# Performance work log

Measured on AMD Instinct MI355X. Metric: run time of the kernel, lower is better.

## Reference

```python
import jax, jax.numpy as jnp
import numpy as np

D_STATE = 512
D_MODEL = 512
BATCH = 8
SEQ = 4096
DT_MIN, DT_MAX = 1e-3, 0.1
LN_EPS = 1e-5


def setup_inputs() -> dict:
    key = jax.random.key(0)
    ks = jax.random.split(key, 4)
    x = jax.random.normal(ks[0], (BATCH, SEQ, D_MODEL), dtype=jnp.float32)
    volatility_scale = jax.random.uniform(ks[1], (BATCH, SEQ, 1), dtype=jnp.float32)
    # parameters (mirroring the torch module's __init__)
    log_lambda_real = jnp.linspace(np.log(DT_MIN), np.log(DT_MAX), D_STATE).astype(jnp.float32)
    log_b = jax.random.uniform(ks[2], (D_STATE, 1), dtype=jnp.float32, minval=-0.5, maxval=0.5)
    c = jax.random.normal(ks[3], (1, D_STATE), dtype=jnp.float32) / np.sqrt(D_STATE)
    log_d = jnp.zeros((1,), jnp.float32)
    ts = np.array([1.0 / 24.0, 1.0, 5.0, 21.0, 63.0], np.float32)
    extra = np.linspace(63.0, 189.0, D_STATE - len(ts), dtype=np.float32)
    log_step = jnp.log(jnp.asarray(np.concatenate([ts, extra])))
    volatility_gate = jnp.ones((D_MODEL,), jnp.float32)
    alpha = jnp.asarray(0.7, jnp.float32)
    ln_weight = jnp.ones((D_STATE,), jnp.float32)
    ln_bias = jnp.zeros((D_STATE,), jnp.float32)
    return dict(x=x, volatility_scale=volatility_scale,
                log_lambda_real=log_lambda_real, log_b=log_b, c=c, log_d=log_d,
                log_step=log_step, volatility_gate=volatility_gate, alpha=alpha,
                ln_weight=ln_weight, ln_bias=ln_bias)


def reference(x, volatility_scale, log_lambda_real, log_b, c, log_d,
              log_step, volatility_gate, alpha, ln_weight, ln_bias):
    lam = -jnp.exp(log_lambda_real)              # [N], negative real poles
    step = jnp.exp(log_step)                     # [N], per-state timescale
    b = jnp.exp(log_b)[:, 0]                     # [N]
    d = jnp.exp(log_d)                           # [1], skip gain
    # bilinear (Tustin) discretization, paired per state
    z = step * lam                               # [N]
    a_disc = (2.0 + z) / (2.0 - z)               # [N]
    b_disc = step * (1.0 + a_disc) * b / 2.0     # [N]
    gate = jax.nn.sigmoid(volatility_gate)       # [D]
    c_vec = c[0]                                 # [N]

    def layer_norm(h):
        mu = jnp.mean(h, axis=-1, keepdims=True)
        var = jnp.var(h, axis=-1, keepdims=True)
        return (h - mu) * jax.lax.rsqrt(var + LN_EPS) * ln_weight + ln_bias

    def scan_step(h, inp):
        x_t, v_t = inp                           # [B,D], [B,1]
        h = a_disc * h + b_disc * x_t            # diagonal SSM update, [B,N]
        h = layer_norm(h)
        h = h / (1.0 + gate * v_t)               # volatility gating
        y_t = jnp.sum(h * c_vec, axis=-1, keepdims=True) + d * x_t  # [B,D]
        return h, y_t

    h0 = jnp.zeros((x.shape[0], a_disc.shape[0]), x.dtype)
    xs = (jnp.swapaxes(x, 0, 1), jnp.swapaxes(volatility_scale, 0, 1))  # time-major
    _, ys = jax.lax.scan(scan_step, h0, xs)      # [S,B,D]
    y = jnp.swapaxes(ys, 0, 1)                   # [B,S,D]
    al = jax.nn.sigmoid(alpha)
    return al * x + (1.0 - al) * y
```

## Files before the change

kernel.cpp:

```cpp
#include <hip/hip_runtime.h>
#include <cstdint>
#include <cstddef>

#define BATCH 8
#define SEQ   4096
#define DS    512
#define JPL   8
#define BLK   8
#define NBLK  (SEQ / BLK)
#define LN_EPS 1e-5f

typedef float v2f __attribute__((ext_vector_type(2)));
typedef float v4f __attribute__((ext_vector_type(4)));

static __device__ __forceinline__ v2f lo2(v4f x) { return __builtin_shufflevector(x, x, 0, 1); }
static __device__ __forceinline__ v2f hi2(v4f x) { return __builtin_shufflevector(x, x, 2, 3); }

#define LGKM0() asm volatile("s_waitcnt lgkmcnt(0)" ::: "memory")
#define BARRIER() __builtin_amdgcn_s_barrier()

template <int CTRL>
__device__ __forceinline__ float dpp_add(float v) {
  int t = __builtin_amdgcn_update_dpp(0, __builtin_bit_cast(int, v), CTRL, 0xF, 0xF, true);
  return v + __builtin_bit_cast(float, t);
}
__device__ __forceinline__ float wave_sum64(float v) {
  v = dpp_add<0x111>(v);
  v = dpp_add<0x112>(v);
  v = dpp_add<0x114>(v);
  v = dpp_add<0x118>(v);
  v = dpp_add<0x142>(v);
  v = dpp_add<0x143>(v);
  return v;
}
__device__ __forceinline__ float bcast63(float v) {
  return __builtin_bit_cast(float, __builtin_amdgcn_readlane(__builtin_bit_cast(int, v), 63));
}

__device__ __forceinline__ void ld16(const float* g, float* l) {
  __builtin_amdgcn_global_load_lds(
      (const __attribute__((address_space(1))) void*)g,
      (__attribute__((address_space(3))) void*)l, 16, 0, 0);
}

__global__ __launch_bounds__(192, 1) void ssm_scan(
    const float* __restrict__ x, const float* __restrict__ vol,
    const float* __restrict__ llr, const float* __restrict__ logb,
    const float* __restrict__ cvec, const float* __restrict__ lstp,
    const float* __restrict__ vgat, const float* __restrict__ lnw,
    const float* __restrict__ lnb, const float* __restrict__ alph,
    const float* __restrict__ logd, float* __restrict__ out)
{
  __shared__ __attribute__((aligned(16))) float X[4][4096];
  __shared__ __attribute__((aligned(16))) float R0[4096], R1[4096];
  __shared__ __attribute__((aligned(16))) float SC0[512], SC1[512];
  __shared__ __attribute__((aligned(16))) float SB0[512], SB1[512];

  const int b    = blockIdx.x;
  const int lane = threadIdx.x & 63;
  const int wid  = threadIdx.x >> 6;

  if (wid == 1) {
    const float* xg = x + (size_t)b * SEQ * DS + lane * JPL;
    float* ob = out + (size_t)b * SEQ * DS;
    float al   = 1.0f / (1.0f + expf(-alph[0]));
    float dd   = expf(logd[0]);
    float coef = __builtin_fmaf(1.0f - al, dd, al);
    float c1   = 1.0f - al;

    auto dma_blk = [&](int blk, float* Xs) {
#pragma unroll
      for (int u = 0; u < BLK; ++u) {
        const float* row = xg + (size_t)(blk * BLK + u) * DS;
        ld16(row,     Xs + u * 512);
        ld16(row + 4, Xs + u * 512 + 256);
      }
    };
    auto out_blk = [&](const float* SCs, const float* Xs, int blk) {
#pragma unroll
      for (int u = 0; u < BLK; ++u) {
        float s  = bcast63(wave_sum64(SCs[u * 64 + lane]));
        float sc = c1 * s;
        v4f xa = *(const v4f*)(Xs + u * 512 + lane * 4);
        v4f xb = *(const v4f*)(Xs + u * 512 + 256 + lane * 4);
        v4f ya = xa * coef + sc;
        v4f yb = xb * coef + sc;
        float* row = ob + (size_t)(blk * BLK + u) * DS + lane * 8;
        *(v4f*)(row)     = ya;
        *(v4f*)(row + 4) = yb;
      }
    };

    dma_blk(0, X[0]);
    dma_blk(1, X[1]);
    asm volatile("s_waitcnt vmcnt(16)" ::: "memory");
    BARRIER();
    dma_blk(2, X[2]);
    asm volatile("s_waitcnt vmcnt(16)" ::: "memory");
    BARRIER();
#pragma unroll 1
    for (int j = 1; j < NBLK; ++j) {
      out_blk((j & 1) ? SC0 : SC1, X[(j - 1) & 3], j - 1);
      LGKM0();
      __builtin_amdgcn_sched_barrier(0);
      if (j + 2 < NBLK) {
        dma_blk(j + 2, X[(j + 2) & 3]);
        asm volatile("s_waitcnt vmcnt(32)" ::: "memory");
      } else if (j + 1 < NBLK) {
        asm volatile("s_waitcnt vmcnt(16)" ::: "memory");
      }
      BARRIER();
    }
    out_blk(SC1, X[(NBLK - 1) & 3], NBLK - 1);
  } else if (wid == 2) {
    v2f gate[4];
#pragma unroll
    for (int j = 0; j < JPL; ++j)
      gate[j >> 1][j & 1] = 1.0f / (1.0f + expf(-vgat[lane * JPL + j]));
    v4f cb0, cb1;
#pragma unroll
    for (int m = 0; m < 4; ++m) {
      int n0 = lane * JPL + m, n1 = lane * JPL + 4 + m;
      cb0[m] = cvec[n0] * lnb[n0];
      cb1[m] = cvec[n1] * lnb[n1];
    }
    const float* vg = vol + (size_t)b * SEQ;

    auto rg_blk = [&](v4f Va, v4f Vb, float* Rs, float* SBs) {
#pragma unroll
      for (int u = 0; u < BLK; ++u) {
        float vt = (u < 4) ? Va[u] : Vb[u - 4];
        v4f r0, r1;
#pragma unroll
        for (int k = 0; k < 4; ++k) {
          v2f den = gate[k] * vt + 1.0f;
          float q0 = __builtin_amdgcn_rcpf(den.x);
          float q1 = __builtin_amdgcn_rcpf(den.y);
          if (k < 2) { r0[2 * k] = q0; r0[2 * k + 1] = q1; }
          else       { r1[2 * (k - 2)] = q0; r1[2 * (k - 2) + 1] = q1; }
        }
        *(v4f*)(Rs + u * 512 + lane * 4)       = r0;
        *(v4f*)(Rs + u * 512 + 256 + lane * 4) = r1;
        v4f md = cb0 * r0;
        md = __builtin_elementwise_fma(cb1, r1, md);
        v2f mh = lo2(md) + hi2(md);
        SBs[u * 64 + lane] = mh.x + mh.y;
      }
    };

    v4f V0a = *(const v4f*)(vg + 0), V0b = *(const v4f*)(vg + 4);
    v4f V1a = *(const v4f*)(vg + 8), V1b = *(const v4f*)(vg + 12);
    rg_blk(V0a, V0b, R0, SB0);
    LGKM0();
    BARRIER();
#pragma unroll 1
    for (int i2 = 0; i2 < NBLK; i2 += 2) {
      if (i2 + 2 < NBLK) {
        V0a = *(const v4f*)(vg + (i2 + 2) * BLK);
        V0b = *(const v4f*)(vg + (i2 + 2) * BLK + 4);
      }
      rg_blk(V1a, V1b, R1, SB1);
      LGKM0();
      BARRIER();
      if (i2 + 3 < NBLK) {
        V1a = *(const v4f*)(vg + (i2 + 3) * BLK);
        V1b = *(const v4f*)(vg + (i2 + 3) * BLK + 4);
      }
      if (i2 + 2 < NBLK) rg_blk(V0a, V0b, R0, SB0);
      LGKM0();
      BARRIER();
    }
  } else {
    v2f bd[4], aw[4], ab[4], cw[4];
#pragma unroll
    for (int j = 0; j < JPL; ++j) {
      int n = lane * JPL + j;
      float lam = -expf(llr[n]);
      float st  = expf(lstp[n]);
      float z   = st * lam;
      float ad  = (2.0f + z) / (2.0f - z);
      float bdv = st * (1.0f + ad) * expf(logb[n]) * 0.5f;
      float wv  = lnw[n], bi = lnb[n], cv = cvec[n];
      bd[j >> 1][j & 1] = bdv;
      aw[j >> 1][j & 1] = ad * wv;
      ab[j >> 1][j & 1] = ad * bi;
      cw[j >> 1][j & 1] = cv * wv;
    }
    v2f hp[4];
#pragma unroll
    for (int k = 0; k < 4; ++k) hp[k] = (v2f){0.0f, 0.0f};

    auto proc_blk = [&](const float* Xs, const float* Rs, const float* SBs, float* SCs) {
#pragma unroll
      for (int u = 0; u < BLK; ++u) {
        v4f xx0 = *(const v4f*)(Xs + u * 512 + lane * 4);
        v4f xx1 = *(const v4f*)(Xs + u * 512 + 256 + lane * 4);
        v4f rr0 = *(const v4f*)(Rs + u * 512 + lane * 4);
        v4f rr1 = *(const v4f*)(Rs + u * 512 + 256 + lane * 4);
        float u3s = SBs[u * 64 + lane];
        v2f xs[4] = {lo2(xx0), hi2(xx0), lo2(xx1), hi2(xx1)};
        v2f rs[4] = {lo2(rr0), hi2(rr0), lo2(rr1), hi2(rr1)};

        v2f hr[4], q[4], abrs[4];
#pragma unroll
        for (int k = 0; k < 4; ++k) {
          hr[k]   = __builtin_elementwise_fma(bd[k], xs[k], hp[k]);
          q[k]    = rs[k] * hr[k];
          abrs[k] = ab[k] * rs[k];
        }
        v2f t01 = hr[0] + hr[1], t23 = hr[2] + hr[3];
        v2f tt  = t01 + t23;
        float s1 = tt.x + tt.y;
        v2f m01 = hr[0] * hr[0];
        m01 = __builtin_elementwise_fma(hr[1], hr[1], m01);
        v2f m23 = hr[2] * hr[2];
        m23 = __builtin_elementwise_fma(hr[3], hr[3], m23);
        v2f mm = m01 + m23;
        float s2 = mm.x + mm.y;

        s1 = bcast63(wave_sum64(s1));
        s2 = bcast63(wave_sum64(s2));
        float mu  = s1 * (1.0f / DS);
        float m2e = __builtin_fmaf(s2, 1.0f / DS, LN_EPS);
        float var = __builtin_fmaf(-mu, mu, m2e);
        float inv = __builtin_amdgcn_rsqf(var);

        v2f muv = {mu, mu}, invv = {inv, inv};
        v2f tv[4];
#pragma unroll
        for (int k = 0; k < 4; ++k)
          tv[k] = __builtin_elementwise_fma(-muv, rs[k], q[k]);
#pragma unroll
        for (int k = 0; k < 4; ++k) {
          v2f sv = aw[k] * tv[k];
          hp[k]  = __builtin_elementwise_fma(invv, sv, abrs[k]);
        }
        v2f u0 = cw[0] * tv[0];
        u0 = __builtin_elementwise_fma(cw[1], tv[1], u0);
        v2f u2 = cw[2] * tv[2];
        u2 = __builtin_elementwise_fma(cw[3], tv[3], u2);
        v2f uu = u0 + u2;
        float u1s = uu.x + uu.y;
        SCs[u * 64 + lane] = __builtin_fmaf(inv, u1s, u3s);
      }
    };

    BARRIER();
#pragma unroll 1
    for (int i4 = 0; i4 < NBLK; i4 += 4) {
      proc_blk(X[0], R0, SB0, SC0); LGKM0(); BARRIER();
      proc_blk(X[1], R1, SB1, SC1); LGKM0(); BARRIER();
      proc_blk(X[2], R0, SB0, SC0); LGKM0(); BARRIER();
      proc_blk(X[3], R1, SB1, SC1); LGKM0(); BARRIER();
    }
  }
}

extern "C" void kernel_launch(void* const* d_in, const int* in_sizes, int n_in,
                              void* d_out, int out_size, void* d_ws, size_t ws_size,
                              hipStream_t stream) {
  const float* x    = (const float*)d_in[0];
  const float* vol  = (const float*)d_in[1];
  const float* llr  = (const float*)d_in[2];
  const float* logb = (const float*)d_in[3];
  const float* cvec = (const float*)d_in[4];
  const float* logd = (const float*)d_in[5];
  const float* lstp = (const float*)d_in[6];
  const float* vgat = (const float*)d_in[7];
  const float* alph = (const float*)d_in[8];
  const float* lnw  = (const float*)d_in[9];
  const float* lnb  = (const float*)d_in[10];
  float* outf = (float*)d_out;

  ssm_scan<<<BATCH, 192, 0, stream>>>(x, vol, llr, logb, cvec, lstp,
                                      vgat, lnw, lnb, alph, logd, outf);
}
```

Measured before the change: 741.1 us.

## Prefetch LDS rows ahead in scan wave and reorder producer DMA issue

The serial LayerNorm-recurrence wave now software-pipelines its shared-memory reads, loading the x, reciprocal-gate and bias rows two timesteps ahead. This is meant to hide LDS latency on the critical sequential chain. The loader wave now issues the next global-to-LDS DMA before writing out the previous block. The gate wave rotates its volatility prefetch registers. Barrier counts stay matched across the three waves, but the consumer loop is no longer unrolled by four and now uses __syncthreads, which may add fence overhead; the prefetch also raises register pressure.

```diff
diff --git a/kernel.cpp b/kernel.cpp
--- a/kernel.cpp
+++ b/kernel.cpp
@@ -17,7 +17,6 @@
 static __device__ __forceinline__ v2f hi2(v4f x) { return __builtin_shufflevector(x, x, 2, 3); }
 
 #define LGKM0() asm volatile("s_waitcnt lgkmcnt(0)" ::: "memory")
-#define BARRIER() __builtin_amdgcn_s_barrier()
 
 template <int CTRL>
 __device__ __forceinline__ float dpp_add(float v) {
@@ -68,7 +67,8 @@
     float coef = __builtin_fmaf(1.0f - al, dd, al);
     float c1   = 1.0f - al;
 
-    auto dma_blk = [&](int blk, float* Xs) {
+    auto dma_blk = [&](int blk) {
+      float* Xs = X[blk & 3];
 #pragma unroll
       for (int u = 0; u < BLK; ++u) {
         const float* row = xg + (size_t)(blk * BLK + u) * DS;
@@ -76,42 +76,39 @@
         ld16(row + 4, Xs + u * 512 + 256);
       }
     };
-    auto out_blk = [&](const float* SCs, const float* Xs, int blk) {
+    auto out_blk = [&](int blk) {
+      const float* SCs = (blk & 1) ? SC1 : SC0;
+      const float* Xs  = X[blk & 3];
 #pragma unroll
       for (int u = 0; u < BLK; ++u) {
         float s  = bcast63(wave_sum64(SCs[u * 64 + lane]));
         float sc = c1 * s;
         v4f xa = *(const v4f*)(Xs + u * 512 + lane * 4);
         v4f xb = *(const v4f*)(Xs + u * 512 + 256 + lane * 4);
-        v4f ya = xa * coef + sc;
-        v4f yb = xb * coef + sc;
         float* row = ob + (size_t)(blk * BLK + u) * DS + lane * 8;
-        *(v4f*)(row)     = ya;
-        *(v4f*)(row + 4) = yb;
-      }
-    };
-
-    dma_blk(0, X[0]);
-    dma_blk(1, X[1]);
+        *(v4f*)(row)     = xa * coef + sc;
+        *(v4f*)(row + 4) = xb * coef + sc;
+      }
+    };
+
+    dma_blk(0);
+    dma_blk(1);
     asm volatile("s_waitcnt vmcnt(16)" ::: "memory");
-    BARRIER();
-    dma_blk(2, X[2]);
-    asm volatile("s_waitcnt vmcnt(16)" ::: "memory");
-    BARRIER();
+    __builtin_amdgcn_s_barrier();
 #pragma unroll 1
-    for (int j = 1; j < NBLK; ++j) {
-      out_blk((j & 1) ? SC0 : SC1, X[(j - 1) & 3], j - 1);
-      LGKM0();
-      __builtin_amdgcn_sched_barrier(0);
-      if (j + 2 < NBLK) {
-        dma_blk(j + 2, X[(j + 2) & 3]);
+    for (int i = 0; i < NBLK; ++i) {
+      if (i + 2 < NBLK) dma_blk(i + 2);
+      if (i >= 1) out_blk(i - 1);
+      if (i == 0) {
+        asm volatile("s_waitcnt vmcnt(16)" ::: "memory");
+      } else if (i + 2 < NBLK) {
         asm volatile("s_waitcnt vmcnt(32)" ::: "memory");
-      } else if (j + 1 < NBLK) {
+      } else {
         asm volatile("s_waitcnt vmcnt(16)" ::: "memory");
       }
-      BARRIER();
-    }
-    out_blk(SC1, X[(NBLK - 1) & 3], NBLK - 1);
+      __builtin_amdgcn_s_barrier();
+    }
+    out_blk(NBLK - 1);
   } else if (wid == 2) {
     v2f gate[4];
 #pragma unroll
@@ -148,27 +145,31 @@
       }
     };
 
-    v4f V0a = *(const v4f*)(vg + 0), V0b = *(const v4f*)(vg + 4);
-    v4f V1a = *(const v4f*)(vg + 8), V1b = *(const v4f*)(vg + 12);
-    rg_blk(V0a, V0b, R0, SB0);
+    v4f V1a = *(const v4f*)(vg + 1 * BLK), V1b = *(const v4f*)(vg + 1 * BLK + 4);
+    v4f V2a = *(const v4f*)(vg + 2 * BLK), V2b = *(const v4f*)(vg + 2 * BLK + 4);
+    {
+      v4f V0a = *(const v4f*)(vg + 0), V0b = *(const v4f*)(vg + 4);
+      rg_blk(V0a, V0b, R0, SB0);
+    }
     LGKM0();
-    BARRIER();
+    __builtin_amdgcn_s_barrier();
 #pragma unroll 1
     for (int i2 = 0; i2 < NBLK; i2 += 2) {
-      if (i2 + 2 < NBLK) {
-        V0a = *(const v4f*)(vg + (i2 + 2) * BLK);
-        V0b = *(const v4f*)(vg + (i2 + 2) * BLK + 4);
-      }
-      rg_blk(V1a, V1b, R1, SB1);
-      LGKM0();
-      BARRIER();
+      if (i2 + 1 < NBLK) rg_blk(V1a, V1b, (i2 & 1) ? R0 : R1,
+                                (i2 & 1) ? SB0 : SB1);
       if (i2 + 3 < NBLK) {
         V1a = *(const v4f*)(vg + (i2 + 3) * BLK);
         V1b = *(const v4f*)(vg + (i2 + 3) * BLK + 4);
       }
-      if (i2 + 2 < NBLK) rg_blk(V0a, V0b, R0, SB0);
       LGKM0();
-      BARRIER();
+      __builtin_amdgcn_s_barrier();
+      if (i2 + 2 < NBLK) rg_blk(V2a, V2b, R0, SB0);
+      if (i2 + 4 < NBLK) {
+        V2a = *(const v4f*)(vg + (i2 + 4) * BLK);
+        V2b = *(const v4f*)(vg + (i2 + 4) * BLK + 4);
+      }
+      LGKM0();
+      __builtin_amdgcn_s_barrier();
     }
   } else {
     v2f bd[4], aw[4], ab[4], cw[4];
@@ -191,13 +192,29 @@
     for (int k = 0; k < 4; ++k) hp[k] = (v2f){0.0f, 0.0f};
 
     auto proc_blk = [&](const float* Xs, const float* Rs, const float* SBs, float* SCs) {
-#pragma unroll
-      for (int u = 0; u < BLK; ++u) {
-        v4f xx0 = *(const v4f*)(Xs + u * 512 + lane * 4);
-        v4f xx1 = *(const v4f*)(Xs + u * 512 + 256 + lane * 4);
-        v4f rr0 = *(const v4f*)(Rs + u * 512 + lane * 4);
-        v4f rr1 = *(const v4f*)(Rs + u * 512 + 256 + lane * 4);
-        float u3s = SBs[u * 64 + lane];
+      v4f px0[2], px1[2], pr0[2], pr1[2];
+      float psb[2];
+#pragma unroll
+      for (int u = 0; u < 2; ++u) {
+        px0[u] = *(const v4f*)(Xs + u * 512 + lane * 4);
+        px1[u] = *(const v4f*)(Xs + u * 512 + 256 + lane * 4);
+        pr0[u] = *(const v4f*)(Rs + u * 512 + lane * 4);
+        pr1[u] = *(const v4f*)(Rs + u * 512 + 256 + lane * 4);
+        psb[u] = SBs[u * 64 + lane];
+      }
+#pragma unroll
+      for (int u = 0; u < BLK; ++u) {
+        const int sl = u & 1;
+        v4f xx0 = px0[sl], xx1 = px1[sl];
+        v4f rr0 = pr0[sl], rr1 = pr1[sl];
+        float u3s = psb[sl];
+        if (u + 2 < BLK) {
+          px0[sl] = *(const v4f*)(Xs + (u + 2) * 512 + lane * 4);
+          px1[sl] = *(const v4f*)(Xs + (u + 2) * 512 + 256 + lane * 4);
+          pr0[sl] = *(const v4f*)(Rs + (u + 2) * 512 + lane * 4);
+          pr1[sl] = *(const v4f*)(Rs + (u + 2) * 512 + 256 + lane * 4);
+          psb[sl] = SBs[(u + 2) * 64 + lane];
+        }
         v2f xs[4] = {lo2(xx0), hi2(xx0), lo2(xx1), hi2(xx1)};
         v2f rs[4] = {lo2(rr0), hi2(rr0), lo2(rr1), hi2(rr1)};
 
@@ -245,13 +262,12 @@
       }
     };
 
-    BARRIER();
+    __syncthreads();
 #pragma unroll 1
-    for (int i4 = 0; i4 < NBLK; i4 += 4) {
-      proc_blk(X[0], R0, SB0, SC0); LGKM0(); BARRIER();
-      proc_blk(X[1], R1, SB1, SC1); LGKM0(); BARRIER();
-      proc_blk(X[2], R0, SB0, SC0); LGKM0(); BARRIER();
-      proc_blk(X[3], R1, SB1, SC1); LGKM0(); BARRIER();
+    for (int i = 0; i < NBLK; ++i) {
+      proc_blk(X[i & 3], (i & 1) ? R1 : R0,
+               (i & 1) ? SB1 : SB0, (i & 1) ? SC1 : SC0);
+      __syncthreads();
     }
   }
 }
```

Measured after the change: 869.3 us. +17.3%, slower.
